# Kernel tuning notes

Hardware: AMD Instinct MI355X
Metric: run time of the kernel (lower is better)

## Reference

```python
import jax, jax.numpy as jnp
import numpy as np

OUT_FEATURES = 11008
IN_FEATURES = 4096
GROUP_SIZE = 16
GROUPS_PER_ROW = IN_FEATURES // GROUP_SIZE
TOTAL_GROUPS = OUT_FEATURES * GROUPS_PER_ROW
PACKED_PER_GROUP = GROUP_SIZE // 2
TOKENS = 4096


def setup_inputs() -> dict:
    key = jax.random.key(0)
    k1, k2, k3, k4 = jax.random.split(key, 4)
    x = jax.random.normal(k1, (TOKENS, IN_FEATURES), dtype=jnp.float32)
    weight_q4 = jax.random.randint(k2, (TOTAL_GROUPS, PACKED_PER_GROUP), 0, 256, dtype=jnp.int32)
    weight_norm = jax.random.uniform(k3, (TOTAL_GROUPS, 1), dtype=jnp.float32).astype(jnp.float16)
    bias = jax.random.normal(k4, (OUT_FEATURES,), dtype=jnp.float32)
    return {"x": x, "weight_q4": weight_q4, "weight_norm": weight_norm, "bias": bias}


def _dequantize(weight_q4, weight_norm):
    # Unpack nibbles, interleaved: even positions = low nibble, odd = high nibble.
    low = weight_q4 & 15
    high = (weight_q4 >> 4) & 15
    q8 = jnp.stack([low, high], axis=-1).reshape(weight_q4.shape[0], -1)  # (TOTAL_GROUPS, GROUP_SIZE)
    norm = weight_norm.astype(jnp.float32)  # (TOTAL_GROUPS, 1)
    w = q8.astype(jnp.float32) / 15.0 * (2.0 * norm) - norm
    return w.reshape(OUT_FEATURES, IN_FEATURES)


def reference(x, weight_q4, weight_norm, bias):
    weight = _dequantize(weight_q4, weight_norm)  # (out, in)
    return jnp.einsum('ti,oi->to', x, weight) + bias
```

## Files before the change

kernel.cpp:

```cpp
#include <hip/hip_runtime.h>
#include <hip/hip_bf16.h>
#include <hip/hip_fp16.h>

#define TOKENS 4096
#define IN_F   4096
#define OUT_F  11008
#define GROUPS_PER_ROW 256
#define TOTAL_GROUPS (OUT_F * GROUPS_PER_ROW)

#define BM 128
#define BN 128
#define BK 32
#define KT_COUNT (IN_F / BK)
#define NBM (TOKENS / BM)
#define NBN (OUT_F / BN)
#define NWG (NBM * NBN)

typedef __bf16 bf16x8 __attribute__((ext_vector_type(8)));
typedef float  f32x4  __attribute__((ext_vector_type(4)));

static __device__ __forceinline__ unsigned short f2bf(float f) {
  unsigned int u = __float_as_uint(f);
  u += 0x7fff + ((u >> 16) & 1);
  return (unsigned short)(u >> 16);
}

static __device__ __forceinline__ void load_lds16(const void* g, void* l) {
  __builtin_amdgcn_global_load_lds(
      (const __attribute__((address_space(1))) void*)g,
      (__attribute__((address_space(3))) void*)l, 16, 0, 0);
}

__global__ void conv_x(const float* __restrict__ x, unsigned short* __restrict__ Xb) {
  int t  = blockIdx.x * 256 + threadIdx.x;
  int m  = t >> 9;
  int c8 = t & 511;
  int k0 = c8 << 3;

  const float4* p = (const float4*)(x + (size_t)m * IN_F + k0);
  float4 a = p[0];
  float4 b = p[1];

  unsigned int w0 = (unsigned int)f2bf(a.x) | ((unsigned int)f2bf(a.y) << 16);
  unsigned int w1 = (unsigned int)f2bf(a.z) | ((unsigned int)f2bf(a.w) << 16);
  unsigned int w2 = (unsigned int)f2bf(b.x) | ((unsigned int)f2bf(b.y) << 16);
  unsigned int w3 = (unsigned int)f2bf(b.z) | ((unsigned int)f2bf(b.w) << 16);

  int mt = m >> 7, r = m & 127;
  int kt = k0 >> 5, c = k0 & 31;
  size_t base = (((size_t)(mt * KT_COUNT + kt)) * 128 + r) * 32 + c;
  *(uint4*)(Xb + base) = make_uint4(w0, w1, w2, w3);
}

__global__ void dequant_w(const int* __restrict__ wq, const float* __restrict__ wn,
                          unsigned short* __restrict__ Wb) {
  int g  = blockIdx.x * 256 + threadIdx.x;
  int o  = g >> 8;
  int gi = g & 255;

  const int4* p = (const int4*)(wq + (size_t)g * 8);
  int4 v0 = p[0];
  int4 v1 = p[1];
  float n = wn[g];
  float s = n * (2.0f / 15.0f);

  int q[8] = {v0.x, v0.y, v0.z, v0.w, v1.x, v1.y, v1.z, v1.w};
  unsigned int w32[8];
#pragma unroll
  for (int j = 0; j < 8; ++j) {
    unsigned short lo = f2bf((float)(q[j] & 15) * s - n);
    unsigned short hi = f2bf((float)((q[j] >> 4) & 15) * s - n);
    w32[j] = (unsigned int)lo | ((unsigned int)hi << 16);
  }

  int k0 = gi << 4;
  int nt = o >> 7, r = o & 127;
  int kt = k0 >> 5, c = k0 & 31;
  size_t base = (((size_t)(nt * KT_COUNT + kt)) * 128 + r) * 32 + c;
  *(uint4*)(Wb + base)     = make_uint4(w32[0], w32[1], w32[2], w32[3]);
  *(uint4*)(Wb + base + 8) = make_uint4(w32[4], w32[5], w32[6], w32[7]);
}

__global__ __launch_bounds__(256) void gemm_bt(
    const unsigned short* __restrict__ Xb, const unsigned short* __restrict__ Wb,
    const float* __restrict__ bias, float* __restrict__ out) {
  __shared__ __align__(16) unsigned short As[2][BM * BK];
  __shared__ __align__(16) unsigned short Bs[2][BN * BK];

  int bid = blockIdx.x;
  int swz = (bid & 7) * (NWG / 8) + (bid >> 3);
  int bm  = swz / NBN;
  int bn  = swz % NBN;

  int tid  = threadIdx.x;
  int lane = tid & 63;
  int wid  = tid >> 6;
  int wr   = wid >> 1, wc = wid & 1;
  int lr   = lane & 15;
  int lk   = (lane >> 4) << 3;

  const char* aTiles = (const char*)Xb + (size_t)bm * KT_COUNT * 8192;
  const char* bTiles = (const char*)Wb + (size_t)bn * KT_COUNT * 8192;
  int soff = wid * 1024 + lane * 16;

#define STAGE(buf_, kt_) do {                                          \
    const char* as_ = aTiles + (size_t)(kt_) * 8192 + soff;            \
    const char* bs_ = bTiles + (size_t)(kt_) * 8192 + soff;            \
    char* ad_ = (char*)&As[buf_][0] + wid * 1024;                      \
    char* bd_ = (char*)&Bs[buf_][0] + wid * 1024;                      \
    load_lds16(as_,        ad_);                                       \
    load_lds16(as_ + 4096, ad_ + 4096);                                \
    load_lds16(bs_,        bd_);                                       \
    load_lds16(bs_ + 4096, bd_ + 4096);                                \
  } while (0)

  f32x4 acc[4][4] = {};

  auto compute = [&](int buf) {
    bf16x8 a[4], b[4];
#pragma unroll
    for (int m = 0; m < 4; ++m)
      a[m] = *(const bf16x8*)&As[buf][(wr * 64 + m * 16 + lr) * BK + lk];
#pragma unroll
    for (int n = 0; n < 4; ++n)
      b[n] = *(const bf16x8*)&Bs[buf][(wc * 64 + n * 16 + lr) * BK + lk];
#pragma unroll
    for (int m = 0; m < 4; ++m)
#pragma unroll
      for (int n = 0; n < 4; ++n)
        acc[m][n] = __builtin_amdgcn_mfma_f32_16x16x32_bf16(a[m], b[n], acc[m][n], 0, 0, 0);
  };

  STAGE(0, 0);
  __syncthreads();
  int cur = 0;
  for (int kt = 0; kt < KT_COUNT - 1; ++kt) {
    STAGE(cur ^ 1, kt + 1);
    compute(cur);
    __syncthreads();
    cur ^= 1;
  }
  compute(cur);

  float bv[4];
#pragma unroll
  for (int n = 0; n < 4; ++n)
    bv[n] = bias[bn * 128 + wc * 64 + n * 16 + lr];

  int row0 = bm * 128 + wr * 64 + ((lane >> 4) << 2);
  int col0 = bn * 128 + wc * 64 + lr;
#pragma unroll
  for (int m = 0; m < 4; ++m) {
#pragma unroll
    for (int n = 0; n < 4; ++n) {
#pragma unroll
      for (int r = 0; r < 4; ++r) {
        int row = row0 + m * 16 + r;
        int col = col0 + n * 16;
        out[(size_t)row * OUT_F + col] = acc[m][n][r] + bv[n];
      }
    }
  }
#undef STAGE
}

extern "C" void kernel_launch(void* const* d_in, const int* in_sizes, int n_in,
                              void* d_out, int out_size, void* d_ws, size_t ws_size,
                              hipStream_t stream) {
  const float*  x    = (const float*)d_in[0];
  const int*    wq   = (const int*)d_in[1];
  const float*  wn   = (const float*)d_in[2];
  const float*  bias = (const float*)d_in[3];
  float*        out  = (float*)d_out;

  unsigned short* Xb = (unsigned short*)d_ws;
  unsigned short* Wb = Xb + (size_t)TOKENS * IN_F;

  conv_x<<<(TOKENS * IN_F / 8) / 256, 256, 0, stream>>>(x, Xb);
  dequant_w<<<TOTAL_GROUPS / 256, 256, 0, stream>>>(wq, wn, Wb);
  gemm_bt<<<NWG, 256, 0, stream>>>(Xb, Wb, bias, out);
}
```

Baseline: 773.5 us.

## Use 256x256 GEMM tiles with swizzled LDS and four-phase pipelined schedule

The GEMM tile grows from 128x128 to 256x256 with BK=64 and 8 waves per block. The conversion kernels now write X and the dequantized weights into an XOR-swizzled pre-tiled layout, so the LDS fragment reads avoid bank conflicts. The main loop is split into four quadrant phases, each interleaving direct global-to-LDS prefetch of upcoming half-tiles with MFMA work, using explicit vmcnt waits, barriers and s_setprio. The aim is to raise arithmetic intensity and hide load latency. The cost is 128KB of LDS per block, heavy register use for 32 accumulators, and a coarser grid that may leave a tail wave.

```diff
diff --git a/kernel.cpp b/kernel.cpp
--- a/kernel.cpp
+++ b/kernel.cpp
@@ -1,6 +1,5 @@
 #include <hip/hip_runtime.h>
 #include <hip/hip_bf16.h>
-#include <hip/hip_fp16.h>
 
 #define TOKENS 4096
 #define IN_F   4096
@@ -8,12 +7,10 @@
 #define GROUPS_PER_ROW 256
 #define TOTAL_GROUPS (OUT_F * GROUPS_PER_ROW)
 
-#define BM 128
-#define BN 128
-#define BK 32
-#define KT_COUNT (IN_F / BK)
-#define NBM (TOKENS / BM)
-#define NBN (OUT_F / BN)
+#define BK 64
+#define KT 64
+#define NBM 16
+#define NBN 43
 #define NWG (NBM * NBN)
 
 typedef __bf16 bf16x8 __attribute__((ext_vector_type(8)));
@@ -31,11 +28,11 @@
       (__attribute__((address_space(3))) void*)l, 16, 0, 0);
 }
 
+
 __global__ void conv_x(const float* __restrict__ x, unsigned short* __restrict__ Xb) {
   int t  = blockIdx.x * 256 + threadIdx.x;
   int m  = t >> 9;
-  int c8 = t & 511;
-  int k0 = c8 << 3;
+  int k0 = (t & 511) << 3;
 
   const float4* p = (const float4*)(x + (size_t)m * IN_F + k0);
   float4 a = p[0];
@@ -46,10 +43,12 @@
   unsigned int w2 = (unsigned int)f2bf(b.x) | ((unsigned int)f2bf(b.y) << 16);
   unsigned int w3 = (unsigned int)f2bf(b.z) | ((unsigned int)f2bf(b.w) << 16);
 
-  int mt = m >> 7, r = m & 127;
-  int kt = k0 >> 5, c = k0 & 31;
-  size_t base = (((size_t)(mt * KT_COUNT + kt)) * 128 + r) * 32 + c;
-  *(uint4*)(Xb + base) = make_uint4(w0, w1, w2, w3);
+  int mt = m >> 8, h = (m >> 7) & 1, r = m & 127;
+  int kt = k0 >> 6;
+  int q  = r * 128 + (k0 & 63) * 2;
+  int qs = q ^ ((q >> 3) & 0x70);
+  char* dst = (char*)Xb + ((((size_t)mt * KT + kt) * 2 + h) * 16384) + qs;
+  *(uint4*)dst = make_uint4(w0, w1, w2, w3);
 }
 
 __global__ void dequant_w(const int* __restrict__ wq, const float* __restrict__ wn,
@@ -64,119 +63,140 @@
   float n = wn[g];
   float s = n * (2.0f / 15.0f);
 
-  int q[8] = {v0.x, v0.y, v0.z, v0.w, v1.x, v1.y, v1.z, v1.w};
+  int q8[8] = {v0.x, v0.y, v0.z, v0.w, v1.x, v1.y, v1.z, v1.w};
   unsigned int w32[8];
 #pragma unroll
   for (int j = 0; j < 8; ++j) {
-    unsigned short lo = f2bf((float)(q[j] & 15) * s - n);
-    unsigned short hi = f2bf((float)((q[j] >> 4) & 15) * s - n);
+    unsigned short lo = f2bf((float)(q8[j] & 15) * s - n);
+    unsigned short hi = f2bf((float)((q8[j] >> 4) & 15) * s - n);
     w32[j] = (unsigned int)lo | ((unsigned int)hi << 16);
   }
 
-  int k0 = gi << 4;
-  int nt = o >> 7, r = o & 127;
-  int kt = k0 >> 5, c = k0 & 31;
-  size_t base = (((size_t)(nt * KT_COUNT + kt)) * 128 + r) * 32 + c;
-  *(uint4*)(Wb + base)     = make_uint4(w32[0], w32[1], w32[2], w32[3]);
-  *(uint4*)(Wb + base + 8) = make_uint4(w32[4], w32[5], w32[6], w32[7]);
-}
-
-__global__ __launch_bounds__(256) void gemm_bt(
+  int nt = o >> 8, h = (o >> 7) & 1, r = o & 127;
+  int kt = gi >> 2;
+  int cb = (gi & 3) * 32;
+  int q0 = r * 128 + cb;
+  int q1 = q0 + 16;
+  int qs0 = q0 ^ ((q0 >> 3) & 0x70);
+  int qs1 = q1 ^ ((q1 >> 3) & 0x70);
+  char* base = (char*)Wb + ((((size_t)nt * KT + kt) * 2 + h) * 16384);
+  *(uint4*)(base + qs0) = make_uint4(w32[0], w32[1], w32[2], w32[3]);
+  *(uint4*)(base + qs1) = make_uint4(w32[4], w32[5], w32[6], w32[7]);
+}
+
+__global__ __launch_bounds__(512, 2) void gemm_bt(
     const unsigned short* __restrict__ Xb, const unsigned short* __restrict__ Wb,
     const float* __restrict__ bias, float* __restrict__ out) {
-  __shared__ __align__(16) unsigned short As[2][BM * BK];
-  __shared__ __align__(16) unsigned short Bs[2][BN * BK];
+  __shared__ __align__(16) char smem[131072];
 
   int bid = blockIdx.x;
-  int swz = (bid & 7) * (NWG / 8) + (bid >> 3);
-  int bm  = swz / NBN;
-  int bn  = swz % NBN;
-
-  int tid  = threadIdx.x;
-  int lane = tid & 63;
-  int wid  = tid >> 6;
-  int wr   = wid >> 1, wc = wid & 1;
-  int lr   = lane & 15;
-  int lk   = (lane >> 4) << 3;
-
-  const char* aTiles = (const char*)Xb + (size_t)bm * KT_COUNT * 8192;
-  const char* bTiles = (const char*)Wb + (size_t)bn * KT_COUNT * 8192;
-  int soff = wid * 1024 + lane * 16;
-
-#define STAGE(buf_, kt_) do {                                          \
-    const char* as_ = aTiles + (size_t)(kt_) * 8192 + soff;            \
-    const char* bs_ = bTiles + (size_t)(kt_) * 8192 + soff;            \
-    char* ad_ = (char*)&As[buf_][0] + wid * 1024;                      \
-    char* bd_ = (char*)&Bs[buf_][0] + wid * 1024;                      \
-    load_lds16(as_,        ad_);                                       \
-    load_lds16(as_ + 4096, ad_ + 4096);                                \
-    load_lds16(bs_,        bd_);                                       \
-    load_lds16(bs_ + 4096, bd_ + 4096);                                \
+  int swzb = (bid & 7) * (NWG / 8) + (bid >> 3);
+  int bm = swzb / NBN, bn = swzb % NBN;
+
+  int tid = threadIdx.x, lane = tid & 63, w = tid >> 6;
+  int wr = w >> 2, wc = w & 3;
+  int lr = lane & 15, gk = lane >> 4;
+
+  const char* aT = (const char*)Xb + (size_t)bm * (KT * 2 * 16384);
+  const char* bT = (const char*)Wb + (size_t)bn * (KT * 2 * 16384);
+  int w1024 = w << 10, lane16 = lane << 4;
+
+  int X = (lane & 7) << 4;
+  int koffs[2] = { ((gk << 4)) ^ X, (64 + (gk << 4)) ^ X };
+  int arow[4], brow[2];
+#pragma unroll
+  for (int m = 0; m < 4; ++m) arow[m] = (wr * 64 + m * 16 + lr) * 128;
+#pragma unroll
+  for (int n = 0; n < 2; ++n) brow[n] = (wc * 32 + n * 16 + lr) * 128;
+
+  auto stage = [&](int buf, int isB, int h, int kt_) {
+    const char* s = (isB ? bT : aT) + ((size_t)kt_ * 2 + h) * 16384 + w1024 + lane16;
+    char* d = smem + (isB ? 65536 : 0) + ((buf << 1) + h) * 16384 + w1024;
+    load_lds16(s, d);
+    load_lds16(s + 8192, d + 8192);
+  };
+
+  f32x4 acc[8][4] = {};
+
+  stage(0, 0, 0, 0); stage(0, 0, 1, 0); stage(0, 1, 0, 0); stage(0, 1, 1, 0);
+  stage(1, 0, 0, 1); stage(1, 1, 0, 1);
+  asm volatile("s_waitcnt vmcnt(4)" ::: "memory");
+  asm volatile("s_barrier" ::: "memory");
+
+#define PHASE(CUR, MH, NH, ISSUE, ENDW) do {                                   \
+    const char* Ab = smem + (((CUR) << 1) + (MH)) * 16384;                     \
+    const char* Bb = smem + 65536 + (((CUR) << 1) + (NH)) * 16384;             \
+    bf16x8 a_[4][2], b_[2][2];                                                 \
+    _Pragma("unroll") for (int m_ = 0; m_ < 4; ++m_)                           \
+      _Pragma("unroll") for (int ks_ = 0; ks_ < 2; ++ks_)                      \
+        a_[m_][ks_] = *(const bf16x8*)(Ab + arow[m_] + koffs[ks_]);            \
+    _Pragma("unroll") for (int n_ = 0; n_ < 2; ++n_)                           \
+      _Pragma("unroll") for (int ks_ = 0; ks_ < 2; ++ks_)                      \
+        b_[n_][ks_] = *(const bf16x8*)(Bb + brow[n_] + koffs[ks_]);            \
+    ISSUE;                                                                     \
+    asm volatile("s_barrier" ::: "memory");                                    \
+    __builtin_amdgcn_s_setprio(1);                                             \
+    _Pragma("unroll") for (int m_ = 0; m_ < 4; ++m_)                           \
+      _Pragma("unroll") for (int n_ = 0; n_ < 2; ++n_)                         \
+        _Pragma("unroll") for (int ks_ = 0; ks_ < 2; ++ks_)                    \
+          acc[(MH) * 4 + m_][(NH) * 2 + n_] =                                  \
+              __builtin_amdgcn_mfma_f32_16x16x32_bf16(                         \
+                  a_[m_][ks_], b_[n_][ks_], acc[(MH) * 4 + m_][(NH) * 2 + n_], \
+                  0, 0, 0);                                                    \
+    __builtin_amdgcn_s_setprio(0);                                             \
+    ENDW;                                                                      \
+    asm volatile("s_barrier" ::: "memory");                                    \
   } while (0)
 
-  f32x4 acc[4][4] = {};
-
-  auto compute = [&](int buf) {
-    bf16x8 a[4], b[4];
+#pragma unroll 2
+  for (int t = 0; t < KT; ++t) {
+    int cur = t & 1, nxt = cur ^ 1;
+    PHASE(cur, 0, 0, { if (t + 1 < KT) stage(nxt, 0, 1, t + 1); }, {});
+    PHASE(cur, 0, 1, { if (t + 1 < KT) stage(nxt, 1, 1, t + 1); }, {});
+    PHASE(cur, 1, 0, { if (t + 2 < KT) stage(cur, 0, 0, t + 2); }, {});
+    PHASE(cur, 1, 1, { if (t + 2 < KT) stage(cur, 1, 0, t + 2); },
+          { if (t >= KT - 2) { asm volatile("s_waitcnt vmcnt(0)" ::: "memory"); }
+            else             { asm volatile("s_waitcnt vmcnt(4)" ::: "memory"); } });
+  }
+#undef PHASE
+
+  float bv[2][2];
+#pragma unroll
+  for (int nh = 0; nh < 2; ++nh)
+#pragma unroll
+    for (int n = 0; n < 2; ++n)
+      bv[nh][n] = bias[bn * 256 + nh * 128 + wc * 32 + n * 16 + lr];
+
+  int colb = bn * 256 + wc * 32 + lr;
+#pragma unroll
+  for (int mh = 0; mh < 2; ++mh)
 #pragma unroll
     for (int m = 0; m < 4; ++m)
-      a[m] = *(const bf16x8*)&As[buf][(wr * 64 + m * 16 + lr) * BK + lk];
-#pragma unroll
-    for (int n = 0; n < 4; ++n)
-      b[n] = *(const bf16x8*)&Bs[buf][(wc * 64 + n * 16 + lr) * BK + lk];
-#pragma unroll
-    for (int m = 0; m < 4; ++m)
-#pragma unroll
-      for (int n = 0; n < 4; ++n)
-        acc[m][n] = __builtin_amdgcn_mfma_f32_16x16x32_bf16(a[m], b[n], acc[m][n], 0, 0, 0);
-  };
-
-  STAGE(0, 0);
-  __syncthreads();
-  int cur = 0;
-  for (int kt = 0; kt < KT_COUNT - 1; ++kt) {
-    STAGE(cur ^ 1, kt + 1);
-    compute(cur);
-    __syncthreads();
-    cur ^= 1;
-  }
-  compute(cur);
-
-  float bv[4];
-#pragma unroll
-  for (int n = 0; n < 4; ++n)
-    bv[n] = bias[bn * 128 + wc * 64 + n * 16 + lr];
-
-  int row0 = bm * 128 + wr * 64 + ((lane >> 4) << 2);
-  int col0 = bn * 128 + wc * 64 + lr;
-#pragma unroll
-  for (int m = 0; m < 4; ++m) {
-#pragma unroll
-    for (int n = 0; n < 4; ++n) {
 #pragma unroll
       for (int r = 0; r < 4; ++r) {
-        int row = row0 + m * 16 + r;
-        int col = col0 + n * 16;
-        out[(size_t)row * OUT_F + col] = acc[m][n][r] + bv[n];
+        int row = bm * 256 + mh * 128 + wr * 64 + m * 16 + (gk << 2) + r;
+        float* po = out + (size_t)row * OUT_F + colb;
+#pragma unroll
+        for (int nh = 0; nh < 2; ++nh)
+#pragma unroll
+          for (int n = 0; n < 2; ++n)
+            po[nh * 128 + n * 16] = acc[mh * 4 + m][nh * 2 + n][r] + bv[nh][n];
       }
-    }
-  }
-#undef STAGE
 }
 
 extern "C" void kernel_launch(void* const* d_in, const int* in_sizes, int n_in,
                               void* d_out, int out_size, void* d_ws, size_t ws_size,
                               hipStream_t stream) {
-  const float*  x    = (const float*)d_in[0];
-  const int*    wq   = (const int*)d_in[1];
-  const float*  wn   = (const float*)d_in[2];
-  const float*  bias = (const float*)d_in[3];
-  float*        out  = (float*)d_out;
+  const float* x    = (const float*)d_in[0];
+  const int*   wq   = (const int*)d_in[1];
+  const float* wn   = (const float*)d_in[2];
+  const float* bias = (const float*)d_in[3];
+  float*       out  = (float*)d_out;
 
   unsigned short* Xb = (unsigned short*)d_ws;
   unsigned short* Wb = Xb + (size_t)TOKENS * IN_F;
 
   conv_x<<<(TOKENS * IN_F / 8) / 256, 256, 0, stream>>>(x, Xb);
   dequant_w<<<TOTAL_GROUPS / 256, 256, 0, stream>>>(wq, wn, Wb);
-  gemm_bt<<<NWG, 256, 0, stream>>>(Xb, Wb, bias, out);
-}
+  gemm_bt<<<NWG, 512, 0, stream>>>(Xb, Wb, bias, out);
+}
```

Result: faster. 657.8 us (-15.0%).
